# Performance work log

Hardware: AMD Instinct MI355X
Metric: run time of the kernel (lower is better)

The kernel has to match this reference:

```python
import jax, jax.numpy as jnp
import numpy as np

NUM_GROUPS = 32
EPS = 1e-5

def group_norm(x, weight, bias):
    # x: [B, C, H, W]
    b, c, h, w = x.shape
    g = NUM_GROUPS
    xg = x.reshape(b, g, (c // g) * h * w)
    mean = xg.mean(axis=-1, keepdims=True)
    var = xg.var(axis=-1, keepdims=True)
    xn = ((xg - mean) * jax.lax.rsqrt(var + EPS)).reshape(b, c, h, w)
    return xn * weight[None, :, None, None] + bias[None, :, None, None]

def setup_inputs() -> dict:
    key = jax.random.key(0)
    ks = jax.random.split(key, 4)
    B, C, H, W = 4, 256, 64, 64
    x = jax.random.normal(ks[0], (B, C, H, W), dtype=jnp.float32)
    gn_weight = jnp.ones((C,), dtype=jnp.float32)
    gn_bias = jnp.zeros((C,), dtype=jnp.float32)
    # 1x1 conv == linear over channel dim; init ~ kaiming-uniform-ish scale
    qkv_weight = jax.random.normal(ks[1], (3 * C, C), dtype=jnp.float32) / np.sqrt(C)
    qkv_bias = jnp.zeros((3 * C,), dtype=jnp.float32)
    out_weight = jax.random.normal(ks[2], (C, C), dtype=jnp.float32) / np.sqrt(C)
    out_bias = jnp.zeros((C,), dtype=jnp.float32)
    return {"x": x, "gn_weight": gn_weight, "gn_bias": gn_bias,
            "qkv_weight": qkv_weight, "qkv_bias": qkv_bias,
            "out_weight": out_weight, "out_bias": out_bias}

def reference(x, gn_weight, gn_bias, qkv_weight, qkv_bias, out_weight, out_bias):
    b, c, h, w = x.shape
    n = h * w
    xn = group_norm(x, gn_weight, gn_bias)
    # 1x1 conv QKV projection: [B, 3C, H, W]
    qkv = jnp.einsum('bchw,oc->bohw', xn, qkv_weight) + qkv_bias[None, :, None, None]
    q, k, v = jnp.split(qkv, 3, axis=1)
    q = q.transpose(0, 2, 3, 1).reshape(b, n, c)   # [B, N, C]
    k = k.reshape(b, c, n)                         # [B, C, N]
    v = v.transpose(0, 2, 3, 1).reshape(b, n, c)   # [B, N, C]
    scores = jnp.einsum('bnc,bcm->bnm', q, k) * (c ** -0.5)  # [B, N, N]
    attn = jax.nn.softmax(scores, axis=-1)
    out = jnp.einsum('bnm,bmc->bnc', attn, v)      # [B, N, C]
    out = out.reshape(b, h, w, c).transpose(0, 3, 1, 2)  # [B, C, H, W]
    out = jnp.einsum('bchw,oc->bohw', out, out_weight) + out_bias[None, :, None, None]
    return out + x
```

## Files before the change

### kernel.cpp

```cpp
#include <hip/hip_runtime.h>
#include <math.h>

#define B_   4
#define C_   256
#define G_   32
#define CPG  8
#define N_   4096
#define NPG  (CPG * N_)
#define EPS  1e-5f
#define SCALE 0.0625f

typedef __attribute__((ext_vector_type(8)))  __bf16 bf16x8;
typedef __attribute__((ext_vector_type(4)))  __bf16 bf16x4;
typedef __attribute__((ext_vector_type(16))) float  f32x16;

__global__ __launch_bounds__(256) void gn_stats_kernel(const float* __restrict__ x,
                                                       float* __restrict__ part) {
    int bid = blockIdx.x;
    int bg = bid >> 2, seg = bid & 3;
    const float4* xp4 = (const float4*)(x + (size_t)bg * NPG) + seg * 2048;
    int tid = threadIdx.x;

    float s = 0.f, ss = 0.f;
    for (int i = tid; i < 2048; i += 256) {
        float4 t = xp4[i];
        s  += t.x + t.y + t.z + t.w;
        ss += t.x * t.x + t.y * t.y + t.z * t.z + t.w * t.w;
    }
    #pragma unroll
    for (int off = 32; off; off >>= 1) {
        s  += __shfl_xor(s, off, 64);
        ss += __shfl_xor(ss, off, 64);
    }
    __shared__ float rs[2][4];
    int wave = tid >> 6, lane = tid & 63;
    if (lane == 0) { rs[0][wave] = s; rs[1][wave] = ss; }
    __syncthreads();
    if (tid == 0) {
        part[bid * 2]     = rs[0][0] + rs[0][1] + rs[0][2] + rs[0][3];
        part[bid * 2 + 1] = rs[1][0] + rs[1][1] + rs[1][2] + rs[1][3];
    }
}

__global__ __launch_bounds__(256) void gn_apply_kernel(const float* __restrict__ x,
                                                       const float* __restrict__ w,
                                                       const float* __restrict__ bia,
                                                       const float* __restrict__ part,
                                                       __bf16* __restrict__ xnb) {
    int bid = blockIdx.x;
    int bg = bid >> 4, seg = bid & 15;
    int b = bg >> 5, g = bg & 31;
    float s  = part[(bg * 4 + 0) * 2] + part[(bg * 4 + 1) * 2]
             + part[(bg * 4 + 2) * 2] + part[(bg * 4 + 3) * 2];
    float ss = part[(bg * 4 + 0) * 2 + 1] + part[(bg * 4 + 1) * 2 + 1]
             + part[(bg * 4 + 2) * 2 + 1] + part[(bg * 4 + 3) * 2 + 1];
    float mean = s / (float)NPG;
    float var  = ss / (float)NPG - mean * mean;
    float rstd = rsqrtf(var + EPS);

    const float* xp = x + (size_t)bg * NPG;
    int n = seg * 256 + threadIdx.x;

    bf16x8 pk;
    #pragma unroll
    for (int cc = 0; cc < 8; cc++) {
        float sc = rstd * w[g * CPG + cc];
        float sh = bia[g * CPG + cc] - mean * sc;
        pk[cc] = (__bf16)(xp[(size_t)cc * N_ + n] * sc + sh);
    }
    size_t idx = ((((size_t)(b * 128 + (n >> 5)) * 16 + (g >> 1)) * 2 + (g & 1))
                  * 32 + (n & 31)) * 8;
    *(bf16x8*)(xnb + idx) = pk;
}

__global__ __launch_bounds__(256) void qkv_kernel(const __bf16* __restrict__ xnb,
                                                  const float* __restrict__ W,
                                                  const float* __restrict__ bias,
                                                  __bf16* __restrict__ q,
                                                  __bf16* __restrict__ k,
                                                  __bf16* __restrict__ v) {
    int b = blockIdx.z, ot = blockIdx.y, nc = blockIdx.x;
    int tid = threadIdx.x, wv = tid >> 6, lane = tid & 63;
    int n31 = lane & 31, q2 = lane >> 5;
    int B0 = ot * 128 + wv * 32;

    bf16x8 wf[16];
    const float* wp = W + (size_t)(B0 + n31) * C_;
    #pragma unroll
    for (int ks = 0; ks < 16; ks++) {
        float4 t0 = *(const float4*)(wp + ks * 16 + q2 * 8);
        float4 t1 = *(const float4*)(wp + ks * 16 + q2 * 8 + 4);
        bf16x8 f;
        f[0] = (__bf16)t0.x; f[1] = (__bf16)t0.y; f[2] = (__bf16)t0.z; f[3] = (__bf16)t0.w;
        f[4] = (__bf16)t1.x; f[5] = (__bf16)t1.y; f[6] = (__bf16)t1.z; f[7] = (__bf16)t1.w;
        wf[ks] = f;
    }

    float bv[16], bvv = 0.f;
    if (ot < 4) {
        #pragma unroll
        for (int gI = 0; gI < 4; gI++)
            #pragma unroll
            for (int j = 0; j < 4; j++)
                bv[gI * 4 + j] = bias[B0 + gI * 8 + 4 * q2 + j];
    } else {
        bvv = bias[B0 + n31];
    }

    const __bf16* xb = xnb + (size_t)b * 128 * 8192;

    for (int t = 0; t < 4; t++) {
        int nt = nc * 4 + t;
        const __bf16* xg = xb + (size_t)nt * 8192 + q2 * 256 + n31 * 8;
        bf16x8 xf[16];
        #pragma unroll
        for (int ks = 0; ks < 16; ks++) xf[ks] = *(const bf16x8*)(xg + ks * 512);

        f32x16 acc;
        #pragma unroll
        for (int i = 0; i < 16; i++) acc[i] = 0.f;
        if (ot < 4) {
            #pragma unroll
            for (int ks = 0; ks < 16; ks++)
                acc = __builtin_amdgcn_mfma_f32_32x32x16_bf16(wf[ks], xf[ks], acc, 0, 0, 0);
        } else {
            #pragma unroll
            for (int ks = 0; ks < 16; ks++)
                acc = __builtin_amdgcn_mfma_f32_32x32x16_bf16(xf[ks], wf[ks], acc, 0, 0, 0);
        }

        if (ot < 4) {
            int ocb = (ot < 2) ? B0 : (B0 - 256);
            __bf16* dst = (ot < 2) ? q : k;
            bool isq = (ot < 2);
            #pragma unroll
            for (int gI = 0; gI < 4; gI++) {
                bf16x4 pk;
                #pragma unroll
                for (int j = 0; j < 4; j++) {
                    float y = acc[gI * 4 + j] + bv[gI * 4 + j];
                    if (isq) y *= SCALE;
                    pk[j] = (__bf16)y;
                }
                size_t idx = ((((size_t)(b * 128 + nt) * 16 + ((ocb >> 4) + (gI >> 1))) * 2
                               + (gI & 1)) * 32 + n31) * 8 + 4 * q2;
                *(bf16x4*)(dst + idx) = pk;
            }
        } else {
            int ocb = B0 - 512;
            #pragma unroll
            for (int gI = 0; gI < 4; gI++) {
                bf16x4 pk;
                #pragma unroll
                for (int j = 0; j < 4; j++)
                    pk[j] = (__bf16)(acc[gI * 4 + j] + bvv);
                size_t idx = (((((size_t)(b * 128 + nt) * 2 + (gI >> 1)) * 2 + (gI & 1)) * 8
                               + (ocb >> 5)) * 32 + n31) * 8 + 4 * q2;
                *(bf16x4*)(v + idx) = pk;
            }
        }
    }
}

#define PSTR 68

__global__ __launch_bounds__(512, 2) void attn_kernel(const __bf16* __restrict__ q,
                                                      const __bf16* __restrict__ k,
                                                      const __bf16* __restrict__ v,
                                                      float* __restrict__ ao0,
                                                      float* __restrict__ ao1,
                                                      float* __restrict__ l0,
                                                      float* __restrict__ l1) {
    __shared__ __bf16 k_lds[2][16384];
    __shared__ __bf16 p_lds[2][128 * PSTR];
    __shared__ float  l_lds[128];

    int bid   = blockIdx.x;
    int xcd   = bid & 7;
    int b     = xcd >> 1;
    int split = xcd & 1;
    int qt    = bid >> 3;
    int n0    = qt * 128;

    int tid = threadIdx.x;
    int wid = tid >> 6, lane = tid & 63;
    int n31 = lane & 31, q2 = lane >> 5;

    if (tid < 128) l_lds[tid] = 0.f;

    const size_t BSTR = (size_t)N_ * C_;
    const __bf16* kbase = k + (size_t)b * BSTR + (size_t)split * 524288;
    const __bf16* vbase = v + (size_t)b * BSTR + (size_t)split * 524288
                          + (size_t)q2 * 2048 + n31 * 8;

    if (wid < 4) {
        int kt = wid & 1;
        int rh = wid >> 1;
        bf16x8 qfA[16], qfB[16];
        const __bf16* qgA = q + (((size_t)(b * 128 + qt * 4 + 2 * rh) * 32 + q2) * 32 + n31) * 8;
        #pragma unroll
        for (int ks = 0; ks < 16; ks++) {
            qfA[ks] = *(const bf16x8*)(qgA + ks * 512);
            qfB[ks] = *(const bf16x8*)(qgA + 8192 + ks * 512);
        }
        float lA = 0.f, lB = 0.f;

        for (int ch = 0; ch < 32; ch++) {
            __syncthreads();
            const __bf16* klds = &k_lds[ch & 1][kt * 8192];
            __bf16* pbuf = p_lds[ch & 1];

            f32x16 sA, sB;
            #pragma unroll
            for (int i = 0; i < 16; i++) { sA[i] = 0.f; sB[i] = 0.f; }
            #pragma unroll
            for (int ks = 0; ks < 16; ks++) {
                bf16x8 kf = *(const bf16x8*)(klds + ks * 512 + lane * 8);
                sA = __builtin_amdgcn_mfma_f32_32x32x16_bf16(kf, qfA[ks], sA, 0, 0, 0);
                sB = __builtin_amdgcn_mfma_f32_32x32x16_bf16(kf, qfB[ks], sB, 0, 0, 0);
            }
            #pragma unroll
            for (int g = 0; g < 4; g++) {
                bf16x4 pwA, pwB;
                #pragma unroll
                for (int j = 0; j < 4; j++) {
                    float pa = __expf(sA[g * 4 + j]);
                    float pb = __expf(sB[g * 4 + j]);
                    lA += pa; lB += pb;
                    pwA[j] = (__bf16)pa; pwB[j] = (__bf16)pb;
                }
                *(bf16x4*)(pbuf + ((2 * rh) * 32 + n31) * PSTR + kt * 32 + 8 * g + 4 * q2) = pwA;
                *(bf16x4*)(pbuf + ((2 * rh + 1) * 32 + n31) * PSTR + kt * 32 + 8 * g + 4 * q2) = pwB;
            }
        }
        atomicAdd(&l_lds[rh * 64 + n31], lA);
        atomicAdd(&l_lds[rh * 64 + 32 + n31], lB);
        __syncthreads();
        if (tid < 128) {
            float* lp = split ? l1 : l0;
            lp[(size_t)b * N_ + n0 + tid] = l_lds[tid];
        }
    } else {
        int cw = wid - 4;
        f32x16 o_acc[2][4];
        #pragma unroll
        for (int ct = 0; ct < 2; ct++)
            #pragma unroll
            for (int rt = 0; rt < 4; rt++)
                #pragma unroll
                for (int i = 0; i < 16; i++) o_acc[ct][rt][i] = 0.f;

        {
            const __bf16* src = kbase + cw * 4096 + lane * 8;
            __bf16* dst = &k_lds[0][cw * 4096];
            #pragma unroll
            for (int i = 0; i < 8; i++)
                __builtin_amdgcn_global_load_lds(
                    (const __attribute__((address_space(1))) void*)(src + i * 512),
                    (__attribute__((address_space(3))) void*)(dst + i * 512), 16, 0, 0);
        }

        for (int ch = 0; ch < 32; ch++) {
            __syncthreads();
            bf16x8 vf[4][2];
            if (ch > 0) {
                #pragma unroll
                for (int ks4 = 0; ks4 < 4; ks4++)
                    #pragma unroll
                    for (int ct = 0; ct < 2; ct++) {
                        size_t off = (size_t)((ch - 1) * 2 + (ks4 >> 1)) * 8192
                                   + (size_t)(ks4 & 1) * 4096 + (cw * 2 + ct) * 256;
                        vf[ks4][ct] = *(const bf16x8*)(vbase + off);
                    }
            }
            if (ch + 1 < 32) {
                const __bf16* src = kbase + (size_t)(ch + 1) * 16384 + cw * 4096 + lane * 8;
                __bf16* dst = &k_lds[(ch + 1) & 1][cw * 4096];
                #pragma unroll
                for (int i = 0; i < 8; i++)
                    __builtin_amdgcn_global_load_lds(
                        (const __attribute__((address_space(1))) void*)(src + i * 512),
                        (__attribute__((address_space(3))) void*)(dst + i * 512), 16, 0, 0);
            }
            if (ch > 0) {
                const __bf16* pbuf = p_lds[(ch - 1) & 1];
                #pragma unroll
                for (int rt = 0; rt < 4; rt++) {
                    const __bf16* pb = pbuf + (rt * 32 + n31) * PSTR + q2 * 8;
                    #pragma unroll
                    for (int ks4 = 0; ks4 < 4; ks4++) {
                        bf16x8 pf = *(const bf16x8*)(pb + ks4 * 16);
                        o_acc[0][rt] = __builtin_amdgcn_mfma_f32_32x32x16_bf16(vf[ks4][0], pf, o_acc[0][rt], 0, 0, 0);
                        o_acc[1][rt] = __builtin_amdgcn_mfma_f32_32x32x16_bf16(vf[ks4][1], pf, o_acc[1][rt], 0, 0, 0);
                    }
                }
            }
        }
        __syncthreads();
        {
            bf16x8 vf[4][2];
            #pragma unroll
            for (int ks4 = 0; ks4 < 4; ks4++)
                #pragma unroll
                for (int ct = 0; ct < 2; ct++) {
                    size_t off = (size_t)(31 * 2 + (ks4 >> 1)) * 8192
                               + (size_t)(ks4 & 1) * 4096 + (cw * 2 + ct) * 256;
                    vf[ks4][ct] = *(const bf16x8*)(vbase + off);
                }
            const __bf16* pbuf = p_lds[1];
            #pragma unroll
            for (int rt = 0; rt < 4; rt++) {
                const __bf16* pb = pbuf + (rt * 32 + n31) * PSTR + q2 * 8;
                #pragma unroll
                for (int ks4 = 0; ks4 < 4; ks4++) {
                    bf16x8 pf = *(const bf16x8*)(pb + ks4 * 16);
                    o_acc[0][rt] = __builtin_amdgcn_mfma_f32_32x32x16_bf16(vf[ks4][0], pf, o_acc[0][rt], 0, 0, 0);
                    o_acc[1][rt] = __builtin_amdgcn_mfma_f32_32x32x16_bf16(vf[ks4][1], pf, o_acc[1][rt], 0, 0, 0);
                }
            }
        }
        float* aop = split ? ao1 : ao0;
        #pragma unroll
        for (int ct = 0; ct < 2; ct++)
            #pragma unroll
            for (int rt = 0; rt < 4; rt++)
                #pragma unroll
                for (int g = 0; g < 4; g++) {
                    float4 st;
                    st.x = o_acc[ct][rt][g * 4 + 0];
                    st.y = o_acc[ct][rt][g * 4 + 1];
                    st.z = o_acc[ct][rt][g * 4 + 2];
                    st.w = o_acc[ct][rt][g * 4 + 3];
                    size_t idx = ((((((size_t)(b * 32 + qt) * 4 + cw) * 2 + ct) * 4 + rt)
                                   * 4 + g) * 2 + q2) * 128 + n31 * 4;
                    *(float4*)(aop + idx) = st;
                }
    }
}

__global__ __launch_bounds__(256) void proj_kernel(const float* __restrict__ ao0,
                                                   const float* __restrict__ ao1,
                                                   const float* __restrict__ l0p,
                                                   const float* __restrict__ l1p,
                                                   const float* __restrict__ W2,
                                                   const float* __restrict__ bias,
                                                   const float* __restrict__ x,
                                                   float* __restrict__ out) {
    int b = blockIdx.z, ot = blockIdx.y, nc = blockIdx.x;
    int tid = threadIdx.x, wv = tid >> 6, lane = tid & 63;
    int n31 = lane & 31, q2 = lane >> 5;
    int B0 = ot * 128 + wv * 32;

    bf16x8 wf[16];
    const float* wp = W2 + (size_t)(B0 + n31) * C_;
    #pragma unroll
    for (int ks = 0; ks < 16; ks++) {
        float4 t0 = *(const float4*)(wp + ks * 16 + q2 * 8);
        float4 t1 = *(const float4*)(wp + ks * 16 + q2 * 8 + 4);
        bf16x8 f;
        f[0] = (__bf16)t0.x; f[1] = (__bf16)t0.y; f[2] = (__bf16)t0.z; f[3] = (__bf16)t0.w;
        f[4] = (__bf16)t1.x; f[5] = (__bf16)t1.y; f[6] = (__bf16)t1.z; f[7] = (__bf16)t1.w;
        wf[ks] = f;
    }
    float bv[16];
    #pragma unroll
    for (int r = 0; r < 16; r++) bv[r] = bias[B0 + (r & 3) + 8 * (r >> 2) + 4 * q2];

    for (int t = 0; t < 4; t++) {
        int nt = nc * 4 + t;
        int qt = nt >> 2, rtile = nt & 3;
        int n = nt * 32 + n31;
        float inv = 1.0f / (l0p[(size_t)b * N_ + n] + l1p[(size_t)b * N_ + n]);

        bf16x8 xf[16];
        #pragma unroll
        for (int ks = 0; ks < 16; ks++) {
            int oct = ks * 2 + q2;
            int cw = oct >> 3, ct = (oct >> 2) & 1, ga = oct & 3;
            size_t base = ((((((size_t)(b * 32 + qt) * 4 + cw) * 2 + ct) * 4 + rtile)
                            * 4 + ga) * 2) * 128 + n31 * 4;
            float4 a0 = *(const float4*)(ao0 + base);
            float4 b0 = *(const float4*)(ao0 + base + 128);
            float4 a1 = *(const float4*)(ao1 + base);
            float4 b1 = *(const float4*)(ao1 + base + 128);
            bf16x8 f;
            f[0] = (__bf16)((a0.x + a1.x) * inv);
            f[1] = (__bf16)((a0.y + a1.y) * inv);
            f[2] = (__bf16)((a0.z + a1.z) * inv);
            f[3] = (__bf16)((a0.w + a1.w) * inv);
            f[4] = (__bf16)((b0.x + b1.x) * inv);
            f[5] = (__bf16)((b0.y + b1.y) * inv);
            f[6] = (__bf16)((b0.z + b1.z) * inv);
            f[7] = (__bf16)((b0.w + b1.w) * inv);
            xf[ks] = f;
        }

        f32x16 acc;
        #pragma unroll
        for (int i = 0; i < 16; i++) acc[i] = 0.f;
        #pragma unroll
        for (int ks = 0; ks < 16; ks++)
            acc = __builtin_amdgcn_mfma_f32_32x32x16_bf16(wf[ks], xf[ks], acc, 0, 0, 0);

        #pragma unroll
        for (int r = 0; r < 16; r++) {
            int o = B0 + (r & 3) + 8 * (r >> 2) + 4 * q2;
            size_t idx = ((size_t)(b * C_ + o)) * N_ + nt * 32 + n31;
            out[idx] = acc[r] + bv[r] + x[idx];
        }
    }
}

extern "C" void kernel_launch(void* const* d_in, const int* in_sizes, int n_in,
                              void* d_out, int out_size, void* d_ws, size_t ws_size,
                              hipStream_t stream) {
    const float* x     = (const float*)d_in[0];
    const float* gn_w  = (const float*)d_in[1];
    const float* gn_b  = (const float*)d_in[2];
    const float* qkv_w = (const float*)d_in[3];
    const float* qkv_b = (const float*)d_in[4];
    const float* out_w = (const float*)d_in[5];
    const float* out_b = (const float*)d_in[6];
    float* out = (float*)d_out;

    const size_t SZ = (size_t)B_ * C_ * N_;
    char* base = (char*)d_ws;
    float*  ao0 = (float*)base;
    float*  ao1 = (float*)(base + SZ * 4);
    __bf16* xnb = (__bf16*)base;
    __bf16* qb  = (__bf16*)(base + 2 * SZ * 4);
    __bf16* kb  = qb + SZ;
    __bf16* vb  = kb + SZ;
    float*  l0  = (float*)(base + 2 * SZ * 4 + 3 * SZ * 2);
    float*  l1  = l0 + B_ * N_;
    float*  part = l1 + B_ * N_;

    gn_stats_kernel<<<dim3(512), 256, 0, stream>>>(x, part);
    gn_apply_kernel<<<dim3(2048), 256, 0, stream>>>(x, gn_w, gn_b, part, xnb);
    qkv_kernel<<<dim3(32, 6, B_), 256, 0, stream>>>(xnb, qkv_w, qkv_b, qb, kb, vb);
    attn_kernel<<<dim3(256), 512, 0, stream>>>(qb, kb, vb, ao0, ao1, l0, l1);
    proj_kernel<<<dim3(32, 2, B_), 256, 0, stream>>>(ao0, ao1, l0, l1, out_w, out_b, x, out);
}
```

Measured before the change: 240.8 us.

## Halve attention query tile and read K directly from global, doubling blocks

The attention kernel now processes 64 query rows per block instead of 128 and launches 512 blocks. K is no longer staged through LDS with async global-to-LDS copies; the score waves read K fragments straight from global memory. Register use drops (one score accumulator, fewer output accumulators), and launch bounds are raised to allow four blocks per CU. This is meant to improve occupancy and latency hiding, at the cost of each K and V tile being reloaded for twice as many query tiles, which raises global/L2 traffic. The proj kernel's indexing is updated to the new output layout.

```diff
diff --git a/kernel.cpp b/kernel.cpp
--- a/kernel.cpp
+++ b/kernel.cpp
@@ -164,166 +164,143 @@
 
 #define PSTR 68
 
-__global__ __launch_bounds__(512, 2) void attn_kernel(const __bf16* __restrict__ q,
+__global__ __launch_bounds__(512, 4) void attn_kernel(const __bf16* __restrict__ q,
                                                       const __bf16* __restrict__ k,
                                                       const __bf16* __restrict__ v,
                                                       float* __restrict__ ao0,
                                                       float* __restrict__ ao1,
                                                       float* __restrict__ l0,
                                                       float* __restrict__ l1) {
-    __shared__ __bf16 k_lds[2][16384];
-    __shared__ __bf16 p_lds[2][128 * PSTR];
-    __shared__ float  l_lds[128];
+    __shared__ __bf16 p_lds[2][64 * PSTR];
+    __shared__ float  l_lds[64];
 
     int bid   = blockIdx.x;
     int xcd   = bid & 7;
     int b     = xcd >> 1;
     int split = xcd & 1;
     int qt    = bid >> 3;
-    int n0    = qt * 128;
+    int n0    = qt * 64;
 
     int tid = threadIdx.x;
     int wid = tid >> 6, lane = tid & 63;
     int n31 = lane & 31, q2 = lane >> 5;
 
-    if (tid < 128) l_lds[tid] = 0.f;
+    if (tid < 64) l_lds[tid] = 0.f;
 
     const size_t BSTR = (size_t)N_ * C_;
-    const __bf16* kbase = k + (size_t)b * BSTR + (size_t)split * 524288;
-    const __bf16* vbase = v + (size_t)b * BSTR + (size_t)split * 524288
-                          + (size_t)q2 * 2048 + n31 * 8;
 
     if (wid < 4) {
         int kt = wid & 1;
-        int rh = wid >> 1;
-        bf16x8 qfA[16], qfB[16];
-        const __bf16* qgA = q + (((size_t)(b * 128 + qt * 4 + 2 * rh) * 32 + q2) * 32 + n31) * 8;
-        #pragma unroll
-        for (int ks = 0; ks < 16; ks++) {
-            qfA[ks] = *(const bf16x8*)(qgA + ks * 512);
-            qfB[ks] = *(const bf16x8*)(qgA + 8192 + ks * 512);
-        }
-        float lA = 0.f, lB = 0.f;
+        int rt = wid >> 1;
+        const __bf16* qg = q + (size_t)(b * 128 + qt * 2 + rt) * 8192
+                           + q2 * 256 + n31 * 8;
+        bf16x8 qf[16];
+        #pragma unroll
+        for (int ks = 0; ks < 16; ks++) qf[ks] = *(const bf16x8*)(qg + ks * 512);
+
+        const __bf16* kbase = k + (size_t)(b * 128 + split * 64 + kt) * 8192
+                              + q2 * 256 + n31 * 8;
+        float l_acc = 0.f;
 
         for (int ch = 0; ch < 32; ch++) {
             __syncthreads();
-            const __bf16* klds = &k_lds[ch & 1][kt * 8192];
+            const __bf16* kg = kbase + (size_t)ch * 16384;
+            f32x16 s;
+            #pragma unroll
+            for (int i = 0; i < 16; i++) s[i] = 0.f;
+            #pragma unroll
+            for (int ks = 0; ks < 16; ks++) {
+                bf16x8 kf = *(const bf16x8*)(kg + ks * 512);
+                s = __builtin_amdgcn_mfma_f32_32x32x16_bf16(kf, qf[ks], s, 0, 0, 0);
+            }
             __bf16* pbuf = p_lds[ch & 1];
-
-            f32x16 sA, sB;
-            #pragma unroll
-            for (int i = 0; i < 16; i++) { sA[i] = 0.f; sB[i] = 0.f; }
-            #pragma unroll
-            for (int ks = 0; ks < 16; ks++) {
-                bf16x8 kf = *(const bf16x8*)(klds + ks * 512 + lane * 8);
-                sA = __builtin_amdgcn_mfma_f32_32x32x16_bf16(kf, qfA[ks], sA, 0, 0, 0);
-                sB = __builtin_amdgcn_mfma_f32_32x32x16_bf16(kf, qfB[ks], sB, 0, 0, 0);
-            }
             #pragma unroll
             for (int g = 0; g < 4; g++) {
-                bf16x4 pwA, pwB;
+                bf16x4 pw;
                 #pragma unroll
                 for (int j = 0; j < 4; j++) {
-                    float pa = __expf(sA[g * 4 + j]);
-                    float pb = __expf(sB[g * 4 + j]);
-                    lA += pa; lB += pb;
-                    pwA[j] = (__bf16)pa; pwB[j] = (__bf16)pb;
-                }
-                *(bf16x4*)(pbuf + ((2 * rh) * 32 + n31) * PSTR + kt * 32 + 8 * g + 4 * q2) = pwA;
-                *(bf16x4*)(pbuf + ((2 * rh + 1) * 32 + n31) * PSTR + kt * 32 + 8 * g + 4 * q2) = pwB;
-            }
-        }
-        atomicAdd(&l_lds[rh * 64 + n31], lA);
-        atomicAdd(&l_lds[rh * 64 + 32 + n31], lB);
+                    float p = __expf(s[g * 4 + j]);
+                    l_acc += p;
+                    pw[j] = (__bf16)p;
+                }
+                *(bf16x4*)(pbuf + (rt * 32 + n31) * PSTR + kt * 32 + 8 * g + 4 * q2) = pw;
+            }
+        }
+        atomicAdd(&l_lds[rt * 32 + n31], l_acc);
         __syncthreads();
-        if (tid < 128) {
+        if (tid < 64) {
             float* lp = split ? l1 : l0;
             lp[(size_t)b * N_ + n0 + tid] = l_lds[tid];
         }
     } else {
         int cw = wid - 4;
-        f32x16 o_acc[2][4];
+        const __bf16* vbase = v + (size_t)b * BSTR + (size_t)split * 524288
+                              + (size_t)q2 * 2048 + n31 * 8;
+        f32x16 o_acc[2][2];
         #pragma unroll
         for (int ct = 0; ct < 2; ct++)
             #pragma unroll
-            for (int rt = 0; rt < 4; rt++)
+            for (int rt = 0; rt < 2; rt++)
                 #pragma unroll
                 for (int i = 0; i < 16; i++) o_acc[ct][rt][i] = 0.f;
-
-        {
-            const __bf16* src = kbase + cw * 4096 + lane * 8;
-            __bf16* dst = &k_lds[0][cw * 4096];
-            #pragma unroll
-            for (int i = 0; i < 8; i++)
-                __builtin_amdgcn_global_load_lds(
-                    (const __attribute__((address_space(1))) void*)(src + i * 512),
-                    (__attribute__((address_space(3))) void*)(dst + i * 512), 16, 0, 0);
-        }
 
         for (int ch = 0; ch < 32; ch++) {
             __syncthreads();
-            bf16x8 vf[4][2];
             if (ch > 0) {
-                #pragma unroll
-                for (int ks4 = 0; ks4 < 4; ks4++)
+                int cc = ch - 1;
+                const __bf16* pbuf = p_lds[cc & 1];
+                #pragma unroll
+                for (int ct = 0; ct < 2; ct++) {
+                    bf16x8 vf[4];
                     #pragma unroll
-                    for (int ct = 0; ct < 2; ct++) {
-                        size_t off = (size_t)((ch - 1) * 2 + (ks4 >> 1)) * 8192
+                    for (int ks4 = 0; ks4 < 4; ks4++) {
+                        size_t off = (size_t)(cc * 2 + (ks4 >> 1)) * 8192
                                    + (size_t)(ks4 & 1) * 4096 + (cw * 2 + ct) * 256;
-                        vf[ks4][ct] = *(const bf16x8*)(vbase + off);
+                        vf[ks4] = *(const bf16x8*)(vbase + off);
                     }
-            }
-            if (ch + 1 < 32) {
-                const __bf16* src = kbase + (size_t)(ch + 1) * 16384 + cw * 4096 + lane * 8;
-                __bf16* dst = &k_lds[(ch + 1) & 1][cw * 4096];
-                #pragma unroll
-                for (int i = 0; i < 8; i++)
-                    __builtin_amdgcn_global_load_lds(
-                        (const __attribute__((address_space(1))) void*)(src + i * 512),
-                        (__attribute__((address_space(3))) void*)(dst + i * 512), 16, 0, 0);
-            }
-            if (ch > 0) {
-                const __bf16* pbuf = p_lds[(ch - 1) & 1];
-                #pragma unroll
-                for (int rt = 0; rt < 4; rt++) {
+                    #pragma unroll
+                    for (int rt = 0; rt < 2; rt++) {
+                        const __bf16* pb = pbuf + (rt * 32 + n31) * PSTR + q2 * 8;
+                        #pragma unroll
+                        for (int ks4 = 0; ks4 < 4; ks4++) {
+                            bf16x8 pf = *(const bf16x8*)(pb + ks4 * 16);
+                            o_acc[ct][rt] = __builtin_amdgcn_mfma_f32_32x32x16_bf16(
+                                vf[ks4], pf, o_acc[ct][rt], 0, 0, 0);
+                        }
+                    }
+                }
+            }
+        }
+        __syncthreads();
+        {
+            int cc = 31;
+            const __bf16* pbuf = p_lds[1];
+            #pragma unroll
+            for (int ct = 0; ct < 2; ct++) {
+                bf16x8 vf[4];
+                #pragma unroll
+                for (int ks4 = 0; ks4 < 4; ks4++) {
+                    size_t off = (size_t)(cc * 2 + (ks4 >> 1)) * 8192
+                               + (size_t)(ks4 & 1) * 4096 + (cw * 2 + ct) * 256;
+                    vf[ks4] = *(const bf16x8*)(vbase + off);
+                }
+                #pragma unroll
+                for (int rt = 0; rt < 2; rt++) {
                     const __bf16* pb = pbuf + (rt * 32 + n31) * PSTR + q2 * 8;
                     #pragma unroll
                     for (int ks4 = 0; ks4 < 4; ks4++) {
                         bf16x8 pf = *(const bf16x8*)(pb + ks4 * 16);
-                        o_acc[0][rt] = __builtin_amdgcn_mfma_f32_32x32x16_bf16(vf[ks4][0], pf, o_acc[0][rt], 0, 0, 0);
-                        o_acc[1][rt] = __builtin_amdgcn_mfma_f32_32x32x16_bf16(vf[ks4][1], pf, o_acc[1][rt], 0, 0, 0);
+                        o_acc[ct][rt] = __builtin_amdgcn_mfma_f32_32x32x16_bf16(
+                            vf[ks4], pf, o_acc[ct][rt], 0, 0, 0);
                     }
                 }
             }
         }
-        __syncthreads();
-        {
-            bf16x8 vf[4][2];
-            #pragma unroll
-            for (int ks4 = 0; ks4 < 4; ks4++)
-                #pragma unroll
-                for (int ct = 0; ct < 2; ct++) {
-                    size_t off = (size_t)(31 * 2 + (ks4 >> 1)) * 8192
-                               + (size_t)(ks4 & 1) * 4096 + (cw * 2 + ct) * 256;
-                    vf[ks4][ct] = *(const bf16x8*)(vbase + off);
-                }
-            const __bf16* pbuf = p_lds[1];
-            #pragma unroll
-            for (int rt = 0; rt < 4; rt++) {
-                const __bf16* pb = pbuf + (rt * 32 + n31) * PSTR + q2 * 8;
-                #pragma unroll
-                for (int ks4 = 0; ks4 < 4; ks4++) {
-                    bf16x8 pf = *(const bf16x8*)(pb + ks4 * 16);
-                    o_acc[0][rt] = __builtin_amdgcn_mfma_f32_32x32x16_bf16(vf[ks4][0], pf, o_acc[0][rt], 0, 0, 0);
-                    o_acc[1][rt] = __builtin_amdgcn_mfma_f32_32x32x16_bf16(vf[ks4][1], pf, o_acc[1][rt], 0, 0, 0);
-                }
-            }
-        }
         float* aop = split ? ao1 : ao0;
         #pragma unroll
         for (int ct = 0; ct < 2; ct++)
             #pragma unroll
-            for (int rt = 0; rt < 4; rt++)
+            for (int rt = 0; rt < 2; rt++)
                 #pragma unroll
                 for (int g = 0; g < 4; g++) {
                     float4 st;
@@ -331,7 +308,7 @@
                     st.y = o_acc[ct][rt][g * 4 + 1];
                     st.z = o_acc[ct][rt][g * 4 + 2];
                     st.w = o_acc[ct][rt][g * 4 + 3];
-                    size_t idx = ((((((size_t)(b * 32 + qt) * 4 + cw) * 2 + ct) * 4 + rt)
+                    size_t idx = ((((((size_t)(b * 64 + qt) * 4 + cw) * 2 + ct) * 2 + rt)
                                    * 4 + g) * 2 + q2) * 128 + n31 * 4;
                     *(float4*)(aop + idx) = st;
                 }
@@ -368,7 +345,7 @@
 
     for (int t = 0; t < 4; t++) {
         int nt = nc * 4 + t;
-        int qt = nt >> 2, rtile = nt & 3;
+        int qt = nt >> 1, rtile = nt & 1;
         int n = nt * 32 + n31;
         float inv = 1.0f / (l0p[(size_t)b * N_ + n] + l1p[(size_t)b * N_ + n]);
 
@@ -377,7 +354,7 @@
         for (int ks = 0; ks < 16; ks++) {
             int oct = ks * 2 + q2;
             int cw = oct >> 3, ct = (oct >> 2) & 1, ga = oct & 3;
-            size_t base = ((((((size_t)(b * 32 + qt) * 4 + cw) * 2 + ct) * 4 + rtile)
+            size_t base = ((((((size_t)(b * 64 + qt) * 4 + cw) * 2 + ct) * 2 + rtile)
                             * 4 + ga) * 2) * 128 + n31 * 4;
             float4 a0 = *(const float4*)(ao0 + base);
             float4 b0 = *(const float4*)(ao0 + base + 128);
@@ -438,6 +415,6 @@
     gn_stats_kernel<<<dim3(512), 256, 0, stream>>>(x, part);
     gn_apply_kernel<<<dim3(2048), 256, 0, stream>>>(x, gn_w, gn_b, part, xnb);
     qkv_kernel<<<dim3(32, 6, B_), 256, 0, stream>>>(xnb, qkv_w, qkv_b, qb, kb, vb);
-    attn_kernel<<<dim3(256), 512, 0, stream>>>(qb, kb, vb, ao0, ao1, l0, l1);
+    attn_kernel<<<dim3(512), 512, 0, stream>>>(qb, kb, vb, ao0, ao1, l0, l1);
     proj_kernel<<<dim3(32, 2, B_), 256, 0, stream>>>(ao0, ao1, l0, l1, out_w, out_b, x, out);
 }
```

After: 229.7 us. -4.6%, faster.
